# Performance work log

Hardware: AMD Instinct MI355X
Metric: run time of the kernel (lower is better)

Reference implementation:

```python
import jax, jax.numpy as jnp
import numpy as np

RADIUS = 0.1
NSAMPLE = 64


def ball_query(xyz, new_xyz, pointsnum, radius, nsample):
    """xyz (B,N,2), new_xyz (B,S,2), pointsnum (B,) -> idx (B,S,nsample) int32.
    Mirrors CUDA ball_query: for each query take the first `nsample` point
    indices (in index order) whose squared distance < radius^2 and index <
    pointsnum[b]; slots beyond the number found are padded with the first
    found index (0 if none found)."""
    N = xyz.shape[1]
    # (B,S,N) squared distances
    d2 = jnp.sum((new_xyz[:, :, None, :] - xyz[:, None, :, :]) ** 2, axis=-1)
    valid = jnp.arange(N, dtype=jnp.int32)[None, None, :] < pointsnum[:, None, None]
    mask = (d2 < radius * radius) & valid
    # key = point index if in ball else N (sentinel); smallest `nsample` keys
    key = jnp.where(mask, jnp.arange(N, dtype=jnp.int32), N)
    neg_small, _ = jax.lax.top_k(-key, nsample)          # largest of -key == smallest keys
    sorted_keys = -neg_small                              # ascending in-ball indices, N-padded
    first = sorted_keys[..., :1]
    pad = jnp.where(first < N, first, 0)
    idx = jnp.where(sorted_keys < N, sorted_keys, pad)
    return idx.astype(jnp.int32)


def group(features, idx):
    """features (B,C,N), idx (B,S,K) -> (B,C,S,K)."""
    return jax.vmap(lambda f, i: f[:, i])(features, idx)


def setup_inputs() -> dict:
    key = jax.random.key(0)
    k1, k2, k3 = jax.random.split(key, 3)
    B, N, S, C = 4, 16384, 2048, 64
    xyz = jax.random.uniform(k1, (B, N, 2), dtype=jnp.float32)
    new_xyz = jax.random.uniform(k2, (B, S, 2), dtype=jnp.float32)
    features = jax.random.normal(k3, (B, C, N), dtype=jnp.float32)
    pointsnum = jnp.full((B,), N, dtype=jnp.int32)
    return {"xyz": xyz, "new_xyz": new_xyz, "features": features, "pointsnum": pointsnum}


def reference(xyz, new_xyz, features, pointsnum):
    # QueryAndGroup(radius=RADIUS, nsample=NSAMPLE, use_xyz=True)
    idx = ball_query(xyz, new_xyz, pointsnum, RADIUS, NSAMPLE)  # (B,S,K) int32
    xyz_t = jnp.transpose(xyz, (0, 2, 1))                        # (B,2,N)
    grouped_xyz = group(xyz_t, idx)                              # (B,2,S,K)
    grouped_xyz = grouped_xyz - jnp.transpose(new_xyz, (0, 2, 1))[..., None]
    grouped_features = group(features, idx)                      # (B,C,S,K)
    new_features = jnp.concatenate([grouped_xyz, grouped_features], axis=1)  # (B,2+C,S,K)
    return new_features
```

## Files before the change

kernel.cpp:

```cpp
#include <hip/hip_runtime.h>
#include <stdint.h>

#define B 4
#define N 16384
#define S 2048
#define C 64
#define K 64
#define OC 66
#define R2 0.01f

__global__ __launch_bounds__(256) void transpose_kernel(const float* __restrict__ f,
                                                        float* __restrict__ ft) {
    __shared__ float tile[64 * 65];
    const int n0 = blockIdx.x * 64;
    const int b  = blockIdx.y;
    const int t  = threadIdx.x;

    const int nl = t & 63, cl = t >> 6;
    #pragma unroll
    for (int cc = cl; cc < 64; cc += 4) {
        tile[cc * 65 + nl] = f[((size_t)b * C + cc) * N + n0 + nl];
    }
    __syncthreads();

    const int cl2 = t & 63, nl2 = t >> 6;
    #pragma unroll
    for (int nn = nl2; nn < 64; nn += 4) {
        ft[((size_t)b * N + n0 + nn) * C + cl2] = tile[cl2 * 65 + nn];
    }
}

template <bool USE_T>
__global__ __launch_bounds__(256) void qag_kernel(const float* __restrict__ xyz,
                                                  const float* __restrict__ new_xyz,
                                                  const float* __restrict__ feat,
                                                  const float* __restrict__ ft,
                                                  const int* __restrict__ pointsnum,
                                                  float* __restrict__ out) {
    __shared__ int s_idx[4][K];

    const int t    = threadIdx.x;
    const int lane = t & 63;
    const int w    = t >> 6;
    const int q    = blockIdx.x * 4 + w;
    const int b    = q >> 11;
    const int s    = q & (S - 1);

    const float qx = new_xyz[(size_t)q * 2 + 0];
    const float qy = new_xyz[(size_t)q * 2 + 1];
    const float* __restrict__ xb = xyz + (size_t)b * N * 2;

    int pn = pointsnum[b];
    pn = pn < 0 ? 0 : (pn > N ? N : pn);
    int cnt = 0;
    for (int base = 0; base < pn && cnt < K; base += 256) {
        float2 p[4];
        #pragma unroll
        for (int u = 0; u < 4; ++u) {
            int i  = base + u * 64 + lane;
            int ic = i < N ? i : N - 1;
            p[u] = *(const float2*)&xb[(size_t)ic * 2];
        }
        #pragma unroll
        for (int u = 0; u < 4; ++u) {
            const int i = base + u * 64 + lane;
            bool ok = false;
            if (i < pn) {
                const float dx = __fsub_rn(qx, p[u].x);
                const float dy = __fsub_rn(qy, p[u].y);
                const float d2 = __fadd_rn(__fmul_rn(dx, dx), __fmul_rn(dy, dy));
                ok = d2 < R2;
            }
            const unsigned long long m = __ballot(ok);
            if (ok) {
                const int pos = cnt + __popcll(m & ((1ull << lane) - 1ull));
                if (pos < K) s_idx[w][pos] = i;
            }
            cnt += __popcll(m);
        }
    }
    const int found = cnt < K ? cnt : K;
    const int first = (found > 0) ? s_idx[w][0] : 0;
    const int id    = (lane < found) ? s_idx[w][lane] : first;

    const size_t SK    = (size_t)S * K;
    const size_t obase = ((size_t)b * OC) * SK + (size_t)s * K + lane;

    const float2 pxy = *(const float2*)&xb[(size_t)id * 2];

    float4 v[16];
    if (USE_T) {
        const float* __restrict__ row = ft + ((size_t)b * N + id) * C;
        #pragma unroll
        for (int g = 0; g < 16; ++g) v[g] = *(const float4*)&row[g * 4];
    } else {
        const float* __restrict__ fb = feat + (size_t)b * C * N;
        #pragma unroll
        for (int g = 0; g < 16; ++g) {
            v[g].x = fb[(size_t)(4 * g + 0) * N + id];
            v[g].y = fb[(size_t)(4 * g + 1) * N + id];
            v[g].z = fb[(size_t)(4 * g + 2) * N + id];
            v[g].w = fb[(size_t)(4 * g + 3) * N + id];
        }
    }

    out[obase]      = pxy.x - qx;
    out[obase + SK] = pxy.y - qy;
    #pragma unroll
    for (int g = 0; g < 16; ++g) {
        out[obase + (size_t)(2 + 4 * g + 0) * SK] = v[g].x;
        out[obase + (size_t)(2 + 4 * g + 1) * SK] = v[g].y;
        out[obase + (size_t)(2 + 4 * g + 2) * SK] = v[g].z;
        out[obase + (size_t)(2 + 4 * g + 3) * SK] = v[g].w;
    }
}

extern "C" void kernel_launch(void* const* d_in, const int* in_sizes, int n_in,
                              void* d_out, int out_size, void* d_ws, size_t ws_size,
                              hipStream_t stream) {
    const float* xyz       = (const float*)d_in[0];
    const float* new_xyz   = (const float*)d_in[1];
    const float* feat      = (const float*)d_in[2];
    const int*   pointsnum = (const int*)d_in[3];
    float*       out       = (float*)d_out;

    const size_t need = (size_t)B * N * C * sizeof(float);
    if (ws_size >= need) {
        float* ft = (float*)d_ws;
        transpose_kernel<<<dim3(N / 64, B), 256, 0, stream>>>(feat, ft);
        qag_kernel<true><<<B * S / 4, 256, 0, stream>>>(xyz, new_xyz, feat, ft, pointsnum, out);
    } else {
        qag_kernel<false><<<B * S / 4, 256, 0, stream>>>(xyz, new_xyz, feat, nullptr, pointsnum, out);
    }
}
```

Before: 60.73 us.

## Stage gathered features through LDS for 16-byte nontemporal output stores

The feature output writes now pass through an LDS tile in chunks of 16 channels. Each wave then writes one channel across all four queries of the block as contiguous 16-byte nontemporal vector stores, instead of scalar per-lane stores spread over strided channel planes. The transpose input loads and the xyz-offset stores also become nontemporal, so streaming data does not pollute the cache. The cost is extra LDS traffic and eight block-wide barriers per block, which couple the four waves after their independent ball-query loops.

```diff
diff --git a/kernel.cpp b/kernel.cpp
--- a/kernel.cpp
+++ b/kernel.cpp
@@ -9,6 +9,8 @@
 #define OC 66
 #define R2 0.01f
 
+typedef float f32x4 __attribute__((ext_vector_type(4)));
+
 __global__ __launch_bounds__(256) void transpose_kernel(const float* __restrict__ f,
                                                         float* __restrict__ ft) {
     __shared__ float tile[64 * 65];
@@ -19,7 +21,7 @@
     const int nl = t & 63, cl = t >> 6;
     #pragma unroll
     for (int cc = cl; cc < 64; cc += 4) {
-        tile[cc * 65 + nl] = f[((size_t)b * C + cc) * N + n0 + nl];
+        tile[cc * 65 + nl] = __builtin_nontemporal_load(&f[((size_t)b * C + cc) * N + n0 + nl]);
     }
     __syncthreads();
 
@@ -37,14 +39,17 @@
                                                   const float* __restrict__ ft,
                                                   const int* __restrict__ pointsnum,
                                                   float* __restrict__ out) {
-    __shared__ int s_idx[4][K];
+    __shared__ int   s_idx[4][K];
+    __shared__ float tile[4][16][K];
 
     const int t    = threadIdx.x;
     const int lane = t & 63;
-    const int w    = t >> 6;
-    const int q    = blockIdx.x * 4 + w;
-    const int b    = q >> 11;
-    const int s    = q & (S - 1);
+    const int wu   = __builtin_amdgcn_readfirstlane(t >> 6);
+    const int q0   = blockIdx.x * 4;
+    const int b    = q0 >> 11;
+    const int s0   = q0 & (S - 1);
+    const int q    = q0 + wu;
+    const int s    = s0 + wu;
 
     const float qx = new_xyz[(size_t)q * 2 + 0];
     const float qy = new_xyz[(size_t)q * 2 + 1];
@@ -74,44 +79,65 @@
             const unsigned long long m = __ballot(ok);
             if (ok) {
                 const int pos = cnt + __popcll(m & ((1ull << lane) - 1ull));
-                if (pos < K) s_idx[w][pos] = i;
+                if (pos < K) s_idx[wu][pos] = i;
             }
             cnt += __popcll(m);
         }
     }
     const int found = cnt < K ? cnt : K;
-    const int first = (found > 0) ? s_idx[w][0] : 0;
-    const int id    = (lane < found) ? s_idx[w][lane] : first;
+    const int first = (found > 0) ? s_idx[wu][0] : 0;
+    const int id    = (lane < found) ? s_idx[wu][lane] : first;
 
-    const size_t SK    = (size_t)S * K;
-    const size_t obase = ((size_t)b * OC) * SK + (size_t)s * K + lane;
-
+    const size_t SK = (size_t)S * K;
     const float2 pxy = *(const float2*)&xb[(size_t)id * 2];
-
-    float4 v[16];
-    if (USE_T) {
-        const float* __restrict__ row = ft + ((size_t)b * N + id) * C;
-        #pragma unroll
-        for (int g = 0; g < 16; ++g) v[g] = *(const float4*)&row[g * 4];
-    } else {
-        const float* __restrict__ fb = feat + (size_t)b * C * N;
-        #pragma unroll
-        for (int g = 0; g < 16; ++g) {
-            v[g].x = fb[(size_t)(4 * g + 0) * N + id];
-            v[g].y = fb[(size_t)(4 * g + 1) * N + id];
-            v[g].z = fb[(size_t)(4 * g + 2) * N + id];
-            v[g].w = fb[(size_t)(4 * g + 3) * N + id];
-        }
+    {
+        float* ob = out + ((size_t)b * OC) * SK + (size_t)s * K;
+        __builtin_nontemporal_store(pxy.x - qx, ob + lane);
+        __builtin_nontemporal_store(pxy.y - qy, ob + SK + lane);
     }
 
-    out[obase]      = pxy.x - qx;
-    out[obase + SK] = pxy.y - qy;
+    const float* __restrict__ row = USE_T ? (ft + ((size_t)b * N + id) * C) : nullptr;
+    const float* __restrict__ fb  = feat + (size_t)b * C * N;
+    const int ql = lane >> 4;
+    const int kq = (lane & 15) * 4;
+
     #pragma unroll
-    for (int g = 0; g < 16; ++g) {
-        out[obase + (size_t)(2 + 4 * g + 0) * SK] = v[g].x;
-        out[obase + (size_t)(2 + 4 * g + 1) * SK] = v[g].y;
-        out[obase + (size_t)(2 + 4 * g + 2) * SK] = v[g].z;
-        out[obase + (size_t)(2 + 4 * g + 3) * SK] = v[g].w;
+    for (int cc = 0; cc < 4; ++cc) {
+        float4 g0, g1, g2, g3;
+        if (USE_T) {
+            const float4* r4 = (const float4*)(row + 16 * cc);
+            g0 = r4[0]; g1 = r4[1]; g2 = r4[2]; g3 = r4[3];
+        } else {
+            const int c0 = 16 * cc;
+            g0.x = fb[(size_t)(c0 +  0) * N + id]; g0.y = fb[(size_t)(c0 +  1) * N + id];
+            g0.z = fb[(size_t)(c0 +  2) * N + id]; g0.w = fb[(size_t)(c0 +  3) * N + id];
+            g1.x = fb[(size_t)(c0 +  4) * N + id]; g1.y = fb[(size_t)(c0 +  5) * N + id];
+            g1.z = fb[(size_t)(c0 +  6) * N + id]; g1.w = fb[(size_t)(c0 +  7) * N + id];
+            g2.x = fb[(size_t)(c0 +  8) * N + id]; g2.y = fb[(size_t)(c0 +  9) * N + id];
+            g2.z = fb[(size_t)(c0 + 10) * N + id]; g2.w = fb[(size_t)(c0 + 11) * N + id];
+            g3.x = fb[(size_t)(c0 + 12) * N + id]; g3.y = fb[(size_t)(c0 + 13) * N + id];
+            g3.z = fb[(size_t)(c0 + 14) * N + id]; g3.w = fb[(size_t)(c0 + 15) * N + id];
+        }
+
+        __syncthreads();
+        tile[wu][ 0][lane] = g0.x; tile[wu][ 1][lane] = g0.y;
+        tile[wu][ 2][lane] = g0.z; tile[wu][ 3][lane] = g0.w;
+        tile[wu][ 4][lane] = g1.x; tile[wu][ 5][lane] = g1.y;
+        tile[wu][ 6][lane] = g1.z; tile[wu][ 7][lane] = g1.w;
+        tile[wu][ 8][lane] = g2.x; tile[wu][ 9][lane] = g2.y;
+        tile[wu][10][lane] = g2.z; tile[wu][11][lane] = g2.w;
+        tile[wu][12][lane] = g3.x; tile[wu][13][lane] = g3.y;
+        tile[wu][14][lane] = g3.z; tile[wu][15][lane] = g3.w;
+        __syncthreads();
+
+        #pragma unroll
+        for (int j = 0; j < 4; ++j) {
+            const int c16 = 4 * wu + j;
+            const int c   = 16 * cc + c16;
+            f32x4 vv = *(const f32x4*)&tile[ql][c16][kq];
+            float* bp = out + ((size_t)b * OC + 2 + c) * SK + (size_t)s0 * K;
+            __builtin_nontemporal_store(vv, ((f32x4*)bp) + lane);
+        }
     }
 }
 
```

Result: no change. 59.56 us (-1.9%).
